# Optimization experiments

Hardware: AMD Instinct MI355X
Metric: run time of the kernel (lower is better)

## Reference

```python
import jax, jax.numpy as jnp
import numpy as np

HEADS = 8

def setup_inputs() -> dict:
    key = jax.random.key(0)
    ks = jax.random.split(key, 10)
    B, S, E = 2, 2048, 512
    q = jax.random.normal(ks[0], (B, S, E), jnp.float32)
    k = jax.random.normal(ks[1], (B, S, E), jnp.float32)
    v = jax.random.normal(ks[2], (B, S, E), jnp.float32)
    mask = jnp.zeros((S, S), jnp.float32)  # additive mask [s_q, s_k]
    scale = 0.02
    Wq = jax.random.normal(ks[3], (E, E), jnp.float32) * scale
    bq = jax.random.normal(ks[4], (E,), jnp.float32) * scale
    Wk = jax.random.normal(ks[5], (E, E), jnp.float32) * scale
    bk = jax.random.normal(ks[6], (E,), jnp.float32) * scale
    Wv = jax.random.normal(ks[7], (E, E), jnp.float32) * scale
    bv = jax.random.normal(ks[8], (E,), jnp.float32) * scale
    return {"q": q, "k": k, "v": v, "mask": mask,
            "Wq": Wq, "bq": bq, "Wk": Wk, "bk": bk, "Wv": Wv, "bv": bv}

def reference(q, k, v, mask, Wq, bq, Wk, bk, Wv, bv):
    H = HEADS
    b, s_q, _ = q.shape
    s_k = k.shape[1]
    s_v = v.shape[1]
    # NOTE: faithful to source: row-major view(b, H, s, -1) WITHOUT transposing
    # seq/head axes first (quirk of the original module).
    K = jnp.swapaxes((k @ Wk.T + bk).reshape(b, H, s_k, -1), 2, 3)  # [b,H,dh,s_k]
    Q = (q @ Wq.T + bq).reshape(b, H, s_q, -1)                      # [b,H,s_q,dh]
    V = (v @ Wv.T + bv).reshape(b, H, s_v, -1)                      # [b,H,s_v,dh]
    # NOTE: original scales by sqrt(K.shape[-1]) AFTER the transpose, i.e. sqrt(s_k)
    scores = (Q @ K) / jnp.sqrt(jnp.asarray(s_k, jnp.float32))      # [b,H,s_q,s_k]
    scores = scores + mask[:s_q, :s_k]
    attn = jax.nn.softmax(scores, axis=-1)
    out = (attn @ V).reshape(b, s_q, -1)  # [b, s_q, e]
    return out
```

## Files before the change

### kernel.cpp

```cpp
#include <hip/hip_runtime.h>


#define SEQ 2048
#define EMB 512
#define DH  64
#define MROWS 4096
#define NROWS 32768
#define L2E 1.4426950408889634f

typedef float  v4f __attribute__((ext_vector_type(4)));
typedef short  v8s __attribute__((ext_vector_type(8)));
typedef __fp16 v2h __attribute__((ext_vector_type(2)));

static __device__ __forceinline__ unsigned int f2bf(float f) {
    unsigned int u = __float_as_uint(f);
    u += 0x7fffu + ((u >> 16) & 1u);
    return u >> 16;
}
static __device__ __forceinline__ unsigned int pack2(float a, float b) {
    return f2bf(a) | (f2bf(b) << 16);
}
static __device__ __forceinline__ unsigned int packh2(float a, float b) {
    v2h h = __builtin_amdgcn_cvt_pkrtz(a, b);
    return __builtin_bit_cast(unsigned int, h);
}

__global__ __launch_bounds__(256, 3) void proj_kernel(
    const float* __restrict__ q, const float* __restrict__ k, const float* __restrict__ v,
    const float* __restrict__ Wq, const float* __restrict__ bq,
    const float* __restrict__ Wk, const float* __restrict__ bk,
    const float* __restrict__ Wv, const float* __restrict__ bv,
    const float* __restrict__ mask,
    unsigned short* __restrict__ Qbf, unsigned short* __restrict__ Kbf,
    unsigned short* __restrict__ Vbf, float* __restrict__ maskT,
    unsigned int* __restrict__ flags)
{
    __shared__ __align__(16) char smem[27648];
    const int tid = threadIdx.x;

    if (blockIdx.x >= 768) {
        const int mb2 = blockIdx.x - 768;
        const int rb = mb2 >> 5, kt = mb2 & 31;
        float* tile = maskT + ((size_t)rb * 32 + kt) * 8192;
        float4 vals[8];
        bool any = false;
#pragma unroll
        for (int i = 0; i < 8; ++i) {
            int s = tid + i * 256;
            int l  = s & 63;
            int cb = (s >> 6) & 3;
            int g  = (s >> 8) & 1;
            int w2 = (s >> 9) & 3;
            int qd2 = l >> 4, n2 = l & 15;
            vals[i] = *(const float4*)&mask[
                (size_t)(rb * 128 + w2 * 32 + g * 16 + n2) * SEQ + kt * 64 + cb * 16 + qd2 * 4];
            any = any | (vals[i].x != 0.f) | (vals[i].y != 0.f)
                      | (vals[i].z != 0.f) | (vals[i].w != 0.f);
        }
        unsigned int* nzp = (unsigned int*)smem;
        if (tid == 0) *nzp = 0u;
        __syncthreads();
        if (any) *nzp = 1u;
        __syncthreads();
        if (*nzp) {
#pragma unroll
            for (int i = 0; i < 8; ++i) {
                int s = tid + i * 256;
                vals[i].x *= L2E; vals[i].y *= L2E;
                vals[i].z *= L2E; vals[i].w *= L2E;
                *(float4*)&tile[(size_t)s * 4] = vals[i];
            }
            if (tid == 0) atomicOr(&flags[rb], 1u << kt);
        }
        return;
    }

    char* As = smem;
    char* Ws = smem + 9216;

    const int id  = blockIdx.x;
    const int pos = id & 31;
    const int nb  = pos >> 3;
    const int unit = (id >> 5) * 8 + (pos & 7);
    const int mb = unit & 63;
    const int z  = unit >> 6;

    const float* A    = (z == 0) ? q  : (z == 1) ? k  : v;
    const float* W    = (z == 0) ? Wq : (z == 1) ? Wk : Wv;
    const float* bias = (z == 0) ? bq : (z == 1) ? bk : bv;
    unsigned short* Cg = (z == 0) ? Qbf : (z == 1) ? Kbf : Vbf;

    const int w    = tid >> 6;
    const int lane = tid & 63;
    const int qd   = lane >> 4;
    const int n    = lane & 15;
    const int m0 = mb * 64, n0 = nb * 128;

    float4 areg[4], wreg[8];
#pragma unroll
    for (int i = 0; i < 4; ++i) {
        int c = tid + i * 256;
        areg[i] = *(const float4*)&A[(size_t)(m0 + (c >> 4)) * EMB + (c & 15) * 4];
    }
#pragma unroll
    for (int i = 0; i < 8; ++i) {
        int c = tid + i * 256;
        wreg[i] = *(const float4*)&W[(size_t)(n0 + (c >> 4)) * EMB + (c & 15) * 4];
    }

    v4f acc[8];
#pragma unroll
    for (int cb = 0; cb < 8; ++cb) acc[cb] = (v4f)0.f;

#pragma unroll 1
    for (int kt = 0; kt < 8; ++kt) {
        __syncthreads();
#pragma unroll
        for (int i = 0; i < 4; ++i) {
            int c = tid + i * 256;
            uint2 pk = { pack2(areg[i].x, areg[i].y), pack2(areg[i].z, areg[i].w) };
            *(uint2*)&As[(c >> 4) * 144 + (c & 15) * 8] = pk;
        }
#pragma unroll
        for (int i = 0; i < 8; ++i) {
            int c = tid + i * 256;
            uint2 pk = { pack2(wreg[i].x, wreg[i].y), pack2(wreg[i].z, wreg[i].w) };
            *(uint2*)&Ws[(c >> 4) * 144 + (c & 15) * 8] = pk;
        }
        __syncthreads();

        if (kt + 1 < 8) {
#pragma unroll
            for (int i = 0; i < 4; ++i) {
                int c = tid + i * 256;
                areg[i] = *(const float4*)&A[(size_t)(m0 + (c >> 4)) * EMB + (kt+1) * 64 + (c & 15) * 4];
            }
#pragma unroll
            for (int i = 0; i < 8; ++i) {
                int c = tid + i * 256;
                wreg[i] = *(const float4*)&W[(size_t)(n0 + (c >> 4)) * EMB + (kt+1) * 64 + (c & 15) * 4];
            }
        }

#pragma unroll
        for (int ks = 0; ks < 2; ++ks) {
            v8s af = *(const v8s*)&As[(w * 16 + n) * 144 + ks * 64 + qd * 16];
#pragma unroll
            for (int cb = 0; cb < 8; ++cb) {
                v8s bfr = *(const v8s*)&Ws[(cb * 16 + n) * 144 + ks * 64 + qd * 16];
                acc[cb] = __builtin_amdgcn_mfma_f32_16x16x32_bf16(af, bfr, acc[cb], 0, 0, 0);
            }
        }
    }

    const float osc = (z == 0) ? 0.031879357905f : 1.0f;
    float bb[8];
#pragma unroll
    for (int cb = 0; cb < 8; ++cb) bb[cb] = bias[n0 + cb * 16 + n];
#pragma unroll
    for (int cb = 0; cb < 8; ++cb)
#pragma unroll
        for (int r = 0; r < 4; ++r) acc[cb][r] = (acc[cb][r] + bb[cb]) * osc;

    __syncthreads();
    short* Ct = (short*)smem;
#pragma unroll
    for (int cb = 0; cb < 8; ++cb)
#pragma unroll
        for (int r = 0; r < 4; ++r)
            Ct[(w * 16 + qd * 4 + r) * 136 + cb * 16 + n] = (short)f2bf(acc[cb][r]);
    __syncthreads();
    const int rr = tid >> 2, q4 = tid & 3;
#pragma unroll
    for (int i = 0; i < 4; ++i) {
        uint4 t4 = *(const uint4*)&smem[rr * 272 + q4 * 64 + i * 16];
        *(uint4*)&Cg[(size_t)(m0 + rr) * EMB + n0 + q4 * 32 + i * 8] = t4;
    }
}

__global__ __launch_bounds__(256) void frag_kernel(
    const unsigned short* __restrict__ Kbf, const unsigned short* __restrict__ Vbf,
    unsigned short* __restrict__ Kfr, unsigned short* __restrict__ Vfr)
{
    __shared__ unsigned short T[64 * 136];
    const int bh = blockIdx.x, kt = blockIdx.y;
    const int tid = threadIdx.x;

    const unsigned short* Kh = Kbf + (size_t)bh * (SEQ * DH) + (size_t)kt * 64 * DH;
#pragma unroll
    for (int i = 0; i < 2; ++i) {
        int c = tid + i * 256;
        uint4 t4 = *(const uint4*)&Kh[c * 8];
        *(uint4*)&T[(c >> 3) * 136 + (c & 7) * 8] = t4;
    }
    __syncthreads();
    unsigned short* Ko = Kfr + ((size_t)bh * 32 + kt) * 4096;
#pragma unroll
    for (int i = 0; i < 2; ++i) {
        int idx = tid + i * 256;
        int f = idx >> 6, l = idx & 63;
        int ks = f >> 2, cb = f & 3, qd = l >> 4, n = l & 15;
        uint4 t4 = *(const uint4*)&T[(cb * 16 + n) * 136 + ks * 32 + qd * 8];
        *(uint4*)&Ko[idx * 8] = t4;
    }
    __syncthreads();
    const unsigned short* Vh = Vbf + (size_t)bh * (SEQ * DH) + (size_t)kt * 64 * DH;
#pragma unroll
    for (int i = 0; i < 2; ++i) {
        int c = tid + i * 256;
        int s_l = c >> 3, ch = c & 7;
        uint4 t4 = *(const uint4*)&Vh[c * 8];
        const unsigned short* e = (const unsigned short*)&t4;
#pragma unroll
        for (int j = 0; j < 8; ++j)
            T[(ch * 8 + j) * 136 + s_l] = e[j];
    }
    __syncthreads();
    unsigned short* Vo = Vfr + ((size_t)bh * 32 + kt) * 4096;
#pragma unroll
    for (int i = 0; i < 2; ++i) {
        int idx = tid + i * 256;
        int f = idx >> 6, l = idx & 63;
        int ks = f >> 2, cb = f & 3, qd = l >> 4, n = l & 15;
        uint4 t4 = *(const uint4*)&T[(cb * 16 + n) * 136 + ks * 32 + qd * 8];
        *(uint4*)&Vo[idx * 8] = t4;
    }
}

template <int SPLITS>
__global__ __launch_bounds__(256, 6) void attn_kernel(
    const unsigned short* __restrict__ Qbf,
    const unsigned short* __restrict__ Kfr, const unsigned short* __restrict__ Vfr,
    const float* __restrict__ maskT, const float* __restrict__ maskf,
    const unsigned int* __restrict__ flags,
    unsigned short* __restrict__ Opart, float* __restrict__ ml,
    float* __restrict__ out)
{
    __shared__ __align__(16) char smem[17408];
    const int tid  = threadIdx.x;
    const int w    = tid >> 6;
    const int lane = tid & 63;
    const int qd   = lane >> 4;
    const int n    = lane & 15;
    const int a_   = qd & 1;
    const bool diag = (a_ == (qd >> 1));

    const int id = blockIdx.x;
    const int bh = (id & 7) * 2 + ((id >> 3) & 1);
    const int unit = id >> 4;
    const int rb6 = unit & 31;
    const int kq = unit >> 5;
    const int KT0 = kq * (32 / SPLITS), KT1 = KT0 + 32 / SPLITS;

    const unsigned short* Qh  = Qbf + (size_t)bh * (SEQ * DH);
    const unsigned short* Kfh = Kfr + (size_t)bh * 32 * 4096;
    const unsigned short* Vfh = Vfr + (size_t)bh * 32 * 4096;

    const unsigned int fl = (SPLITS > 1) ? flags[rb6 >> 1] : 0u;

    v8s qf[2];
    {
        const size_t qrow = (size_t)(rb6 * 64 + w * 16 + n);
#pragma unroll
        for (int ks = 0; ks < 2; ++ks)
            qf[ks] = *(const v8s*)&Qh[qrow * DH + ks * 32 + qd * 8];
    }

    float l_ = 0.f;
    v4f oacc[4];
#pragma unroll
    for (int cb = 0; cb < 4; ++cb) oacc[cb] = (v4f)0.f;

#pragma unroll 1
    for (int kt = KT0; kt < KT1; ++kt) {
        const unsigned short* Kt = Kfh + (size_t)kt * 4096;
        const unsigned short* Vt = Vfh + (size_t)kt * 4096;

        v4f sacc[4];
        float4 mk[4];
        if (SPLITS > 1) {
            if (fl & (1u << kt)) {
                const float* tileF = maskT + ((size_t)(rb6 >> 1) * 32 + kt) * 8192;
                const int wg = (rb6 & 1) * 4 + w;
#pragma unroll
                for (int cb = 0; cb < 4; ++cb)
                    sacc[cb] = *(const v4f*)&tileF[
                        (size_t)((wg * 4 + cb) * 64 + qd * 16 + n) * 4];
            } else {
#pragma unroll
                for (int cb = 0; cb < 4; ++cb) sacc[cb] = (v4f)0.f;
            }
        } else {
            const size_t mrow = (size_t)(rb6 * 64 + w * 16 + n);
#pragma unroll
            for (int cb = 0; cb < 4; ++cb) {
                mk[cb] = *(const float4*)&maskf[mrow * SEQ + kt * 64 + cb * 16 + qd * 4];
                sacc[cb] = (v4f)0.f;
            }
        }

#pragma unroll
        for (int ks = 0; ks < 2; ++ks)
#pragma unroll
            for (int cb = 0; cb < 4; ++cb) {
                v8s kf = *(const v8s*)&Kt[((ks * 4 + cb) * 64 + lane) * 8];
                sacc[cb] = __builtin_amdgcn_mfma_f32_16x16x32_bf16(kf, qf[ks], sacc[cb], 0, 0, 0);
            }

        v8s pfr[2];
        {
            float rs = 0.f;
            unsigned int O_[4][2];
#pragma unroll
            for (int cb = 0; cb < 4; ++cb) {
                float s0 = sacc[cb][0], s1 = sacc[cb][1];
                float s2 = sacc[cb][2], s3 = sacc[cb][3];
                if (SPLITS == 1) {
                    s0 = fmaf(mk[cb].x, L2E, s0);
                    s1 = fmaf(mk[cb].y, L2E, s1);
                    s2 = fmaf(mk[cb].z, L2E, s2);
                    s3 = fmaf(mk[cb].w, L2E, s3);
                }
                float e0 = __builtin_amdgcn_exp2f(s0);
                float e1 = __builtin_amdgcn_exp2f(s1);
                float e2 = __builtin_amdgcn_exp2f(s2);
                float e3 = __builtin_amdgcn_exp2f(s3);
                rs += (e0 + e1) + (e2 + e3);
                O_[cb][0] = pack2(e0, e1);
                O_[cb][1] = pack2(e2, e3);
            }
            rs += __shfl_xor(rs, 16);
            rs += __shfl_xor(rs, 32);
            l_ += rs;
#pragma unroll
            for (int ks = 0; ks < 2; ++ks) {
                unsigned int t0 = a_ ? O_[2 * ks][0] : O_[2 * ks + 1][0];
                unsigned int t1 = a_ ? O_[2 * ks][1] : O_[2 * ks + 1][1];
                unsigned int r0 = __shfl_xor(t0, 16);
                unsigned int r1 = __shfl_xor(t1, 16);
                unsigned int Z00 = a_ ? r0 : O_[2 * ks][0];
                unsigned int Z01 = a_ ? r1 : O_[2 * ks][1];
                unsigned int Z10 = a_ ? O_[2 * ks + 1][0] : r0;
                unsigned int Z11 = a_ ? O_[2 * ks + 1][1] : r1;
                unsigned int s00 = __shfl_xor(Z00, 48);
                unsigned int s01 = __shfl_xor(Z01, 48);
                unsigned int s10 = __shfl_xor(Z10, 48);
                unsigned int s11 = __shfl_xor(Z11, 48);
                uint4 pw;
                pw.x = diag ? Z00 : s00;
                pw.y = diag ? Z01 : s01;
                pw.z = diag ? Z10 : s10;
                pw.w = diag ? Z11 : s11;
                pfr[ks] = __builtin_bit_cast(v8s, pw);
            }
        }

#pragma unroll
        for (int ks = 0; ks < 2; ++ks)
#pragma unroll
            for (int cb = 0; cb < 4; ++cb) {
                v8s vf = *(const v8s*)&Vt[((ks * 4 + cb) * 64 + lane) * 8];
                oacc[cb] = __builtin_amdgcn_mfma_f32_16x16x32_bf16(vf, pfr[ks], oacc[cb], 0, 0, 0);
            }
    }

    if (SPLITS == 1) {
        const float inv = 1.0f / l_;
#pragma unroll
        for (int cb = 0; cb < 4; ++cb)
#pragma unroll
            for (int r = 0; r < 4; ++r) oacc[cb][r] *= inv;
    } else {
        if (qd == 0) {
            const size_t row = (size_t)bh * SEQ + rb6 * 64 + w * 16 + n;
            ml[(size_t)kq * NROWS + row] = l_;
        }
    }
    __syncthreads();
#pragma unroll
    for (int cb = 0; cb < 4; ++cb)
        *(v4f*)&smem[(w * 16 + n) * 272 + cb * 64 + qd * 16] = oacc[cb];
    __syncthreads();
    const int r_l = tid >> 2, q4 = tid & 3;
    if (SPLITS == 1) {
        float* dst = &out[((size_t)bh * SEQ + rb6 * 64 + r_l) * DH + q4 * 16];
#pragma unroll
        for (int i = 0; i < 4; ++i) {
            float4 t4 = *(const float4*)&smem[r_l * 272 + q4 * 64 + i * 16];
            *(float4*)&dst[i * 4] = t4;
        }
    } else {
        unsigned short* dst = &Opart[((size_t)kq * NROWS + (size_t)bh * SEQ + rb6 * 64 + r_l) * DH + q4 * 16];
#pragma unroll
        for (int i = 0; i < 2; ++i) {
            float4 f0 = *(const float4*)&smem[r_l * 272 + q4 * 64 + i * 32];
            float4 f1 = *(const float4*)&smem[r_l * 272 + q4 * 64 + i * 32 + 16];
            uint4 o = { packh2(f0.x, f0.y), packh2(f0.z, f0.w),
                        packh2(f1.x, f1.y), packh2(f1.z, f1.w) };
            *(uint4*)&dst[i * 8] = o;
        }
    }
}

__global__ __launch_bounds__(256) void combine_kernel(
    const unsigned int* __restrict__ Opart, const float* __restrict__ ml,
    float* __restrict__ out, int splits)
{
    const int tid = threadIdx.x;
    const size_t row = (size_t)blockIdx.x * 16 + (tid >> 4);
    const int d4 = (tid & 15) * 4;
    float denom = 0.f;
    float4 o = make_float4(0.f, 0.f, 0.f, 0.f);
    for (int s = 0; s < splits; ++s) {
        denom += ml[(size_t)s * NROWS + row];
        uint2 u = *(const uint2*)&Opart[((size_t)s * NROWS + row) * 32 + (d4 >> 1)];
        v2h h0 = __builtin_bit_cast(v2h, u.x);
        v2h h1 = __builtin_bit_cast(v2h, u.y);
        o.x += (float)h0.x; o.y += (float)h0.y;
        o.z += (float)h1.x; o.w += (float)h1.y;
    }
    const float inv = 1.0f / denom;
    o.x *= inv; o.y *= inv; o.z *= inv; o.w *= inv;
    *(float4*)&out[row * DH + d4] = o;
}

extern "C" void kernel_launch(void* const* d_in, const int* in_sizes, int n_in,
                              void* d_out, int out_size, void* d_ws, size_t ws_size,
                              hipStream_t stream) {
    const float* q    = (const float*)d_in[0];
    const float* k    = (const float*)d_in[1];
    const float* v    = (const float*)d_in[2];
    const float* mask = (const float*)d_in[3];
    const float* Wq   = (const float*)d_in[4];
    const float* bq   = (const float*)d_in[5];
    const float* Wk   = (const float*)d_in[6];
    const float* bk   = (const float*)d_in[7];
    const float* Wv   = (const float*)d_in[8];
    const float* bv   = (const float*)d_in[9];

    char* ws = (char*)d_ws;
    const size_t MB = 1024 * 1024;
    unsigned short* Qbf   = (unsigned short*)(ws + 0);
    unsigned short* Kbf   = (unsigned short*)(ws + 4 * MB);
    unsigned short* Vfr   = (unsigned short*)(ws + 8 * MB);
    unsigned short* Opart = (unsigned short*)(ws + 12 * MB);
    unsigned short* Vbf   = (unsigned short*)(ws + 12 * MB);
    float*          mlp   = (float*)(ws + 28 * MB);
    unsigned int*   flags = (unsigned int*)(ws + 28 * MB + 512 * 1024);
    float*          maskT = (float*)(ws + 29 * MB);

    const size_t need_split = 49 * MB;
    const bool do_split = ws_size >= need_split;

    if (do_split) {
        unsigned short* Kfr = (unsigned short*)(ws + 45 * MB);
        (void)hipMemsetAsync(flags, 0, 64, stream);
        proj_kernel<<<1280, 256, 0, stream>>>(q, k, v, Wq, bq, Wk, bk, Wv, bv,
                                              mask, Qbf, Kbf, Vbf, maskT, flags);
        dim3 tgrid(16, 32);
        frag_kernel<<<tgrid, 256, 0, stream>>>(Kbf, Vbf, Kfr, Vfr);
        attn_kernel<4><<<2048, 256, 0, stream>>>(Qbf, Kfr, Vfr, maskT, mask, flags,
                                                 Opart, mlp, (float*)d_out);
        combine_kernel<<<NROWS / 16, 256, 0, stream>>>((const unsigned int*)Opart,
                                                       mlp, (float*)d_out, 4);
    } else {
        unsigned short* Kfr = (unsigned short*)(ws + 16 * MB);
        proj_kernel<<<768, 256, 0, stream>>>(q, k, v, Wq, bq, Wk, bk, Wv, bv,
                                             mask, Qbf, Kbf, Vbf, maskT, flags);
        dim3 tgrid(16, 32);
        frag_kernel<<<tgrid, 256, 0, stream>>>(Kbf, Vbf, Kfr, Vfr);
        attn_kernel<1><<<512, 256, 0, stream>>>(Qbf, Kfr, Vfr, maskT, mask, flags,
                                                Opart, mlp, (float*)d_out);
    }
}
```

Measured before the change: 173.1 us.

## Write K directly in fragment layout from projection; use hardware bf16 pack

The projection kernel now scatters the K output straight into the MFMA fragment layout that the attention kernel consumes. This drops the K half of the separate fragment-reordering kernel and its round trip through global memory. The software float-to-bf16 rounding is replaced by the packed v_cvt_pk_bf16_f32 instruction in the staging and epilogue paths. The K stores become scattered 16-byte writes, and the hardware conversion's rounding must match the previous round-to-nearest-even.

```diff
diff --git a/kernel.cpp b/kernel.cpp
--- a/kernel.cpp
+++ b/kernel.cpp
@@ -20,6 +20,11 @@
 static __device__ __forceinline__ unsigned int pack2(float a, float b) {
     return f2bf(a) | (f2bf(b) << 16);
 }
+static __device__ __forceinline__ unsigned int cvtpk(float a, float b) {
+    unsigned int r;
+    asm("v_cvt_pk_bf16_f32 %0, %1, %2" : "=v"(r) : "v"(a), "v"(b));
+    return r;
+}
 static __device__ __forceinline__ unsigned int packh2(float a, float b) {
     v2h h = __builtin_amdgcn_cvt_pkrtz(a, b);
     return __builtin_bit_cast(unsigned int, h);
@@ -31,7 +36,7 @@
     const float* __restrict__ Wk, const float* __restrict__ bk,
     const float* __restrict__ Wv, const float* __restrict__ bv,
     const float* __restrict__ mask,
-    unsigned short* __restrict__ Qbf, unsigned short* __restrict__ Kbf,
+    unsigned short* __restrict__ Qbf, unsigned short* __restrict__ Kfr,
     unsigned short* __restrict__ Vbf, float* __restrict__ maskT,
     unsigned int* __restrict__ flags)
 {
@@ -88,7 +93,7 @@
     const float* A    = (z == 0) ? q  : (z == 1) ? k  : v;
     const float* W    = (z == 0) ? Wq : (z == 1) ? Wk : Wv;
     const float* bias = (z == 0) ? bq : (z == 1) ? bk : bv;
-    unsigned short* Cg = (z == 0) ? Qbf : (z == 1) ? Kbf : Vbf;
+    unsigned short* Cg = (z == 0) ? Qbf : Vbf;
 
     const int w    = tid >> 6;
     const int lane = tid & 63;
@@ -118,13 +123,13 @@
 #pragma unroll
         for (int i = 0; i < 4; ++i) {
             int c = tid + i * 256;
-            uint2 pk = { pack2(areg[i].x, areg[i].y), pack2(areg[i].z, areg[i].w) };
+            uint2 pk = { cvtpk(areg[i].x, areg[i].y), cvtpk(areg[i].z, areg[i].w) };
             *(uint2*)&As[(c >> 4) * 144 + (c & 15) * 8] = pk;
         }
 #pragma unroll
         for (int i = 0; i < 8; ++i) {
             int c = tid + i * 256;
-            uint2 pk = { pack2(wreg[i].x, wreg[i].y), pack2(wreg[i].z, wreg[i].w) };
+            uint2 pk = { cvtpk(wreg[i].x, wreg[i].y), cvtpk(wreg[i].z, wreg[i].w) };
             *(uint2*)&Ws[(c >> 4) * 144 + (c & 15) * 8] = pk;
         }
         __syncthreads();
@@ -167,43 +172,43 @@
 #pragma unroll
     for (int cb = 0; cb < 8; ++cb)
 #pragma unroll
-        for (int r = 0; r < 4; ++r)
-            Ct[(w * 16 + qd * 4 + r) * 136 + cb * 16 + n] = (short)f2bf(acc[cb][r]);
+        for (int r = 0; r < 2; ++r) {
+            unsigned int pk = cvtpk(acc[cb][2*r], acc[cb][2*r+1]);
+            Ct[(w * 16 + qd * 4 + 2*r)     * 136 + cb * 16 + n] = (short)(pk & 0xffffu);
+            Ct[(w * 16 + qd * 4 + 2*r + 1) * 136 + cb * 16 + n] = (short)(pk >> 16);
+        }
     __syncthreads();
     const int rr = tid >> 2, q4 = tid & 3;
-#pragma unroll
-    for (int i = 0; i < 4; ++i) {
-        uint4 t4 = *(const uint4*)&smem[rr * 272 + q4 * 64 + i * 16];
-        *(uint4*)&Cg[(size_t)(m0 + rr) * EMB + n0 + q4 * 32 + i * 8] = t4;
+    if (z == 1) {
+        const int bh = m0 >> 8;
+        const int mm = (m0 & 255) + rr;
+        unsigned short* Kh = Kfr + (size_t)bh * 32 * 4096;
+#pragma unroll
+        for (int i = 0; i < 4; ++i) {
+            uint4 t4 = *(const uint4*)&smem[rr * 272 + q4 * 64 + i * 16];
+            int nn = n0 + q4 * 32 + i * 8;
+            int s  = mm * 8 + (nn >> 6);
+            int kt = s >> 6, sk = s & 63;
+            int dd = nn & 63;
+            int entry = ((dd >> 5) * 4 + (sk >> 4)) * 64 + ((dd & 31) >> 3) * 16 + (sk & 15);
+            *(uint4*)&Kh[(size_t)kt * 4096 + entry * 8] = t4;
+        }
+    } else {
+#pragma unroll
+        for (int i = 0; i < 4; ++i) {
+            uint4 t4 = *(const uint4*)&smem[rr * 272 + q4 * 64 + i * 16];
+            *(uint4*)&Cg[(size_t)(m0 + rr) * EMB + n0 + q4 * 32 + i * 8] = t4;
+        }
     }
 }
 
 __global__ __launch_bounds__(256) void frag_kernel(
-    const unsigned short* __restrict__ Kbf, const unsigned short* __restrict__ Vbf,
-    unsigned short* __restrict__ Kfr, unsigned short* __restrict__ Vfr)
+    const unsigned short* __restrict__ Vbf, unsigned short* __restrict__ Vfr)
 {
     __shared__ unsigned short T[64 * 136];
     const int bh = blockIdx.x, kt = blockIdx.y;
     const int tid = threadIdx.x;
 
-    const unsigned short* Kh = Kbf + (size_t)bh * (SEQ * DH) + (size_t)kt * 64 * DH;
-#pragma unroll
-    for (int i = 0; i < 2; ++i) {
-        int c = tid + i * 256;
-        uint4 t4 = *(const uint4*)&Kh[c * 8];
-        *(uint4*)&T[(c >> 3) * 136 + (c & 7) * 8] = t4;
-    }
-    __syncthreads();
-    unsigned short* Ko = Kfr + ((size_t)bh * 32 + kt) * 4096;
-#pragma unroll
-    for (int i = 0; i < 2; ++i) {
-        int idx = tid + i * 256;
-        int f = idx >> 6, l = idx & 63;
-        int ks = f >> 2, cb = f & 3, qd = l >> 4, n = l & 15;
-        uint4 t4 = *(const uint4*)&T[(cb * 16 + n) * 136 + ks * 32 + qd * 8];
-        *(uint4*)&Ko[idx * 8] = t4;
-    }
-    __syncthreads();
     const unsigned short* Vh = Vbf + (size_t)bh * (SEQ * DH) + (size_t)kt * 64 * DH;
 #pragma unroll
     for (int i = 0; i < 2; ++i) {
@@ -448,6 +453,7 @@
     float*          mlp   = (float*)(ws + 28 * MB);
     unsigned int*   flags = (unsigned int*)(ws + 28 * MB + 512 * 1024);
     float*          maskT = (float*)(ws + 29 * MB);
+    (void)Kbf;
 
     const size_t need_split = 49 * MB;
     const bool do_split = ws_size >= need_split;
@@ -456,9 +462,9 @@
         unsigned short* Kfr = (unsigned short*)(ws + 45 * MB);
         (void)hipMemsetAsync(flags, 0, 64, stream);
         proj_kernel<<<1280, 256, 0, stream>>>(q, k, v, Wq, bq, Wk, bk, Wv, bv,
-                                              mask, Qbf, Kbf, Vbf, maskT, flags);
+                                              mask, Qbf, Kfr, Vbf, maskT, flags);
         dim3 tgrid(16, 32);
-        frag_kernel<<<tgrid, 256, 0, stream>>>(Kbf, Vbf, Kfr, Vfr);
+        frag_kernel<<<tgrid, 256, 0, stream>>>(Vbf, Vfr);
         attn_kernel<4><<<2048, 256, 0, stream>>>(Qbf, Kfr, Vfr, maskT, mask, flags,
                                                  Opart, mlp, (float*)d_out);
         combine_kernel<<<NROWS / 16, 256, 0, stream>>>((const unsigned int*)Opart,
@@ -466,9 +472,9 @@
     } else {
         unsigned short* Kfr = (unsigned short*)(ws + 16 * MB);
         proj_kernel<<<768, 256, 0, stream>>>(q, k, v, Wq, bq, Wk, bk, Wv, bv,
-                                             mask, Qbf, Kbf, Vbf, maskT, flags);
+                                             mask, Qbf, Kfr, Vbf, maskT, flags);
         dim3 tgrid(16, 32);
-        frag_kernel<<<tgrid, 256, 0, stream>>>(Kbf, Vbf, Kfr, Vfr);
+        frag_kernel<<<tgrid, 256, 0, stream>>>(Vbf, Vfr);
         attn_kernel<1><<<512, 256, 0, stream>>>(Qbf, Kfr, Vfr, maskT, mask, flags,
                                                 Opart, mlp, (float*)d_out);
     }
```

After: 171.0 us. Within noise of the previous version (-1.2%).
